# Kernel tuning notes

Hardware: AMD Instinct MI355X
Metric: run time of the kernel (lower is better)

The kernel has to match this reference:

```python
import jax, jax.numpy as jnp
import numpy as np

N = 100000          # nodes
E = 600000          # edges (avg degree ~6, mesh graph)
C_IN = 6            # input features (xyz + normals)
H = 64              # hidden channels per PointTransformerConv
OUT = 10            # out_channels
NEG_SLOPE = 0.01    # F.leaky_relu default slope
IN_DIMS = [C_IN, C_IN + H, C_IN + 2 * H, C_IN + 3 * H]


def _lin(key, fin, fout):
    return jax.random.normal(key, (fin, fout), jnp.float32) / np.float32(np.sqrt(fin))


def setup_inputs() -> dict:
    key = jax.random.key(0)
    ks = jax.random.split(key, 40)
    inp = {
        "x": jax.random.normal(ks[0], (N, C_IN), jnp.float32),
        "edge_index": jax.random.randint(ks[1], (2, E), 0, N, jnp.int32),
    }
    k = 2
    for l, fin in enumerate(IN_DIMS, start=1):
        inp[f"w{l}_lin"] = _lin(ks[k], fin, H); k += 1   # value projection (bias=False)
        inp[f"w{l}_src"] = _lin(ks[k], fin, H); k += 1   # attention src projection
        inp[f"w{l}_dst"] = _lin(ks[k], fin, H); k += 1   # attention dst projection
        inp[f"w{l}_pos"] = _lin(ks[k], fin, H); k += 1   # positional MLP (Linear)
        inp[f"b{l}_pos"] = jnp.zeros((H,), jnp.float32)
    inp["w_mlp1"] = _lin(ks[k], C_IN + 4 * H, H); k += 1
    inp["b_mlp1"] = jnp.zeros((H,), jnp.float32)
    inp["w_mlp2"] = _lin(ks[k], H, OUT); k += 1
    inp["b_mlp2"] = jnp.zeros((OUT,), jnp.float32)
    return inp


def _ptconv(x, src, dst, w_lin, w_src, w_dst, w_pos, b_pos):
    """PointTransformerConv with x serving as both features and positions.
    message = softmax_i(a_dst[i] - a_src[j] + delta_ij) * (h[j] + delta_ij),
    delta_ij = pos_nn(x_i - x_j); sum-aggregated over incoming edges."""
    h = x @ w_lin                                   # [N,H] values
    a_src = x @ w_src                               # [N,H]
    a_dst = x @ w_dst                               # [N,H]
    delta = (x[dst] - x[src]) @ w_pos + b_pos       # [E,H] pos_nn(pos_i - pos_j)
    alpha = a_dst[dst] - a_src[src] + delta         # [E,H] per-edge, per-channel logits
    # numerically stable segment softmax over edges grouped by destination node
    amax = jax.ops.segment_max(alpha, dst, num_segments=N)      # [N,H]
    e = jnp.exp(alpha - amax[dst])                              # [E,H]
    denom = jax.ops.segment_sum(e, dst, num_segments=N)         # [N,H]
    w = e / (denom[dst] + 1e-16)                                # [E,H]
    return jax.ops.segment_sum(w * (h[src] + delta), dst, num_segments=N)  # [N,H]


def _forward(x, edge_index, ps):
    src, dst = edge_index[0], edge_index[1]
    lrelu = lambda v: jnp.where(v > 0, v, NEG_SLOPE * v)
    x1 = _ptconv(x, src, dst, *ps[0])
    x2 = lrelu(_ptconv(jnp.concatenate([x, x1], 1), src, dst, *ps[1]))
    x3 = lrelu(_ptconv(jnp.concatenate([x, x1, x2], 1), src, dst, *ps[2]))
    x4 = lrelu(_ptconv(jnp.concatenate([x, x1, x2, x3], 1), src, dst, *ps[3]))
    out = jnp.concatenate([x, x1, x2, x3, x4], 1)   # [N, 262]
    w_mlp1, b_mlp1, w_mlp2, b_mlp2 = ps[4]
    out = out @ w_mlp1 + b_mlp1                     # dropout = identity (eval mode)
    return out @ w_mlp2 + b_mlp2                    # [N, OUT]


def reference(x, edge_index,
              w1_lin, w1_src, w1_dst, w1_pos, b1_pos,
              w2_lin, w2_src, w2_dst, w2_pos, b2_pos,
              w3_lin, w3_src, w3_dst, w3_pos, b3_pos,
              w4_lin, w4_src, w4_dst, w4_pos, b4_pos,
              w_mlp1, b_mlp1, w_mlp2, b_mlp2):
    ps = [(w1_lin, w1_src, w1_dst, w1_pos, b1_pos),
          (w2_lin, w2_src, w2_dst, w2_pos, b2_pos),
          (w3_lin, w3_src, w3_dst, w3_pos, b3_pos),
          (w4_lin, w4_src, w4_dst, w4_pos, b4_pos),
          (w_mlp1, b_mlp1, w_mlp2, b_mlp2)]
    return _forward(x, edge_index, ps)
```

## Files before the change

### kernel.cpp

```cpp
#include <hip/hip_runtime.h>
#include <hip/hip_fp16.h>

#define NN 100000
#define EE 600000
#define XSB 288
#define SCAN_B 2048
#define LOG2E 1.44269504f

typedef __attribute__((ext_vector_type(8))) short s16x8;
typedef __attribute__((ext_vector_type(4))) float f32x4;

__device__ inline unsigned short f2b(float f) {
    unsigned u = __float_as_uint(f);
    u += 0x7fffu + ((u >> 16) & 1u);
    return (unsigned short)(u >> 16);
}

__device__ inline void accum4(float* d, float* s, const uint4& r) {
    const unsigned* u = (const unsigned*)&r;
#pragma unroll
    for (int ch = 0; ch < 4; ch++) {
        d[ch] += __uint_as_float(u[ch] << 16);
        s[ch] += __uint_as_float(u[ch] & 0xFFFF0000u);
    }
}

__device__ inline void wconv_elem(int idx, int fin,
                                  const float* wlin, const float* wsrc,
                                  const float* wpos, unsigned short* wt) {
    int ks = idx / 6144;
    int rem = idx - ks * 6144;
    int col = rem >> 5, kk = rem & 31;
    int k = ks * 32 + kk;
    float val = 0.f;
    if (k < fin) {
        int m = col >> 6, c = col & 63;
        const float* W = (m == 0) ? wlin : (m == 1) ? wsrc : wpos;
        val = W[k * 64 + c];
    }
    wt[idx] = f2b(val);
}

#define O0 600000
#define O1 606144
#define O2 624576
#define O3 655296
#define O4 698304
#define O5 716736
#define O6 1316736
#define O7 1316800

__global__ __launch_bounds__(256) void k_setup(
    const float* __restrict__ x, const int* __restrict__ ei,
    const float* __restrict__ wl0, const float* __restrict__ ws0, const float* __restrict__ wp0,
    const float* __restrict__ wl1, const float* __restrict__ ws1, const float* __restrict__ wp1,
    const float* __restrict__ wl2, const float* __restrict__ ws2, const float* __restrict__ wp2,
    const float* __restrict__ wl3, const float* __restrict__ ws3, const float* __restrict__ wp3,
    const float* __restrict__ w1,
    unsigned short* __restrict__ xb,
    unsigned short* __restrict__ wt0, unsigned short* __restrict__ wt1,
    unsigned short* __restrict__ wt2, unsigned short* __restrict__ wt3,
    unsigned short* __restrict__ w1t, int* __restrict__ deg,
    unsigned* __restrict__ vgu) {
    int i = blockIdx.x * 256 + threadIdx.x;
    if (i < O0) {
        int n = i / 6, c = i - n * 6;
        xb[(size_t)n * XSB + c] = f2b(x[i]);
    } else if (i < O1) {
        wconv_elem(i - O0, 6, wl0, ws0, wp0, wt0);
    } else if (i < O2) {
        wconv_elem(i - O1, 70, wl1, ws1, wp1, wt1);
    } else if (i < O3) {
        wconv_elem(i - O2, 134, wl2, ws2, wp2, wt2);
    } else if (i < O4) {
        wconv_elem(i - O3, 198, wl3, ws3, wp3, wt3);
    } else if (i < O5) {
        int idx = i - O4;
        int col = idx / 288, k = idx - col * 288;
        w1t[idx] = f2b((k < 262) ? w1[k * 64 + col] : 0.f);
    } else if (i < O6) {
        atomicAdd(&deg[ei[EE + (i - O5)]], 1);
    } else if (i < O7) {
        vgu[(size_t)NN * 64 + (i - O6)] = 0u;
    }
}


__global__ void k_scan1(const int* __restrict__ deg, int* __restrict__ rowptr,
                        int* __restrict__ bsum) {
    __shared__ int sh[256];
    int b = blockIdx.x, t = threadIdx.x;
    int base = b * SCAN_B + t * 8;
    int vals[8];
    int s = 0;
#pragma unroll
    for (int j = 0; j < 8; j++) {
        int i = base + j;
        int d = (i < NN) ? deg[i] : 0;
        s += d;
        vals[j] = s;
    }
    sh[t] = s;
    __syncthreads();
    for (int off = 1; off < 256; off <<= 1) {
        int vv = (t >= off) ? sh[t - off] : 0;
        __syncthreads();
        sh[t] += vv;
        __syncthreads();
    }
    int excl = (t > 0) ? sh[t - 1] : 0;
#pragma unroll
    for (int j = 0; j < 8; j++) {
        int i = base + j;
        if (i < NN) rowptr[i + 1] = vals[j] + excl;
    }
    if (t == 255) bsum[b] = sh[255];
}

__global__ void k_scan3m(const int* __restrict__ deg, int* __restrict__ rowptr,
                         const int* __restrict__ bsum, int* __restrict__ cursor) {
    __shared__ int soff;
    int b = blockIdx.x, t = threadIdx.x;
    if (t < 64) {
        int v = (t < b) ? bsum[t] : 0;
#pragma unroll
        for (int m = 1; m < 64; m <<= 1) v += __shfl_xor(v, m);
        if (t == 0) soff = v;
    }
    __syncthreads();
    int off = soff;
    int base = b * SCAN_B + t * 8;
#pragma unroll
    for (int j = 0; j < 8; j++) {
        int i = base + j;
        if (i < NN) {
            int incl = rowptr[i + 1] + off;
            rowptr[i + 1] = incl;
            cursor[i] = incl - deg[i];
        }
    }
    if (b == 0 && t == 0) rowptr[0] = 0;
}

__global__ void k_scatter(const int* __restrict__ ei, int* __restrict__ cursor,
                          int* __restrict__ csrc) {
    int e = blockIdx.x * 256 + threadIdx.x;
    if (e < EE) {
        int d = ei[EE + e];
        int pos = atomicAdd(&cursor[d], 1);
        csrc[pos] = ei[e];
    }
}


template <int KP>
__global__ __launch_bounds__(256) void k_projm(
    const unsigned short* __restrict__ xb, const unsigned short* __restrict__ wt,
    const float* __restrict__ bpos,
    unsigned* __restrict__ vg, __half* __restrict__ qh) {
    __shared__ short wl[192 * 32];
    const int t = threadIdx.x;
    const int w = t >> 6, l = t & 63;
    const int lo = l & 15, hi = l >> 4;
    const int row_w = blockIdx.x * 128 + w * 32;

    f32x4 acc[2][12];
#pragma unroll
    for (int a = 0; a < 2; a++)
#pragma unroll
        for (int i = 0; i < 12; i++) acc[a][i] = (f32x4)0.f;

    const unsigned short* arow0 = xb + (size_t)(row_w + lo) * XSB;
    const unsigned short* arow1 = xb + (size_t)(row_w + 16 + lo) * XSB;
#pragma unroll
    for (int ks = 0; ks < KP / 32; ks++) {
        __syncthreads();
        {
            const uint4* src = (const uint4*)wt + (size_t)ks * 768;
            uint4* dst = (uint4*)wl;
#pragma unroll
            for (int i = 0; i < 3; i++) {
                int idx = i * 256 + t;
                dst[idx ^ ((idx >> 3) & 7)] = src[idx];
            }
        }
        __syncthreads();
        s16x8 af0 = *(const s16x8*)(arow0 + ks * 32 + hi * 8);
        s16x8 af1 = *(const s16x8*)(arow1 + ks * 32 + hi * 8);
#pragma unroll
        for (int ct = 0; ct < 12; ct++) {
            int ridx = (ct * 16 + lo) * 4 + hi;
            s16x8 bf = *(const s16x8*)&wl[(size_t)(ridx ^ ((ridx >> 3) & 7)) * 8];
            acc[0][ct] = __builtin_amdgcn_mfma_f32_16x16x32_bf16(af0, bf, acc[0][ct], 0, 0, 0);
            acc[1][ct] = __builtin_amdgcn_mfma_f32_16x16x32_bf16(af1, bf, acc[1][ct], 0, 0, 0);
        }
    }

#pragma unroll
    for (int tile = 0; tile < 2; tile++) {
#pragma unroll
        for (int r = 0; r < 4; r++) {
            int node = row_w + tile * 16 + hi * 4 + r;
            if (node < NN) {
#pragma unroll
                for (int j = 0; j < 4; j++) {
                    int c = j * 16 + lo;
                    float h  = acc[tile][0 + j][r];
                    float as = acc[tile][4 + j][r];
                    float p  = acc[tile][8 + j][r];
                    size_t o = (size_t)node * 64 + c;
                    float P = __builtin_amdgcn_exp2f(-(as + p) * LOG2E);
                    vg[o] = (unsigned)f2b(P) | ((unsigned)f2b(P * (h - p)) << 16);
                    qh[o] = __float2half(p + bpos[c]);
                }
            }
        }
    }
}


__global__ __launch_bounds__(256) void k_mlp1f(
    const unsigned short* __restrict__ xb, const unsigned short* __restrict__ w1t,
    const float* __restrict__ b1, const float* __restrict__ w2,
    const float* __restrict__ b2, float* __restrict__ out) {
    __shared__ float w2l[64][10];
    __shared__ float b2l[10];
    __shared__ float b1l[64];
    for (int t = threadIdx.x; t < 714; t += 256) {
        if (t < 640) ((float*)w2l)[t] = w2[t];
        else if (t < 650) b2l[t - 640] = b2[t - 640];
        else b1l[t - 650] = b1[t - 650];
    }
    __syncthreads();

    const int w = threadIdx.x >> 6, l = threadIdx.x & 63;
    const int lo = l & 15, hi = l >> 4;
    const int row_w = blockIdx.x * 256 + w * 64;

    f32x4 acc[4][4];
#pragma unroll
    for (int a = 0; a < 4; a++)
#pragma unroll
        for (int b = 0; b < 4; b++) acc[a][b] = (f32x4)0.f;

#pragma unroll
    for (int ks = 0; ks < 9; ks++) {
        const int k0 = ks * 32 + hi * 8;
        s16x8 bf[4];
#pragma unroll
        for (int ct = 0; ct < 4; ct++)
            bf[ct] = *(const s16x8*)(w1t + (size_t)(ct * 16 + lo) * 288 + k0);
#pragma unroll
        for (int rt = 0; rt < 4; rt++) {
            s16x8 af = *(const s16x8*)(xb + (size_t)(row_w + rt * 16 + lo) * XSB + k0);
#pragma unroll
            for (int ct = 0; ct < 4; ct++)
                acc[rt][ct] = __builtin_amdgcn_mfma_f32_16x16x32_bf16(af, bf[ct], acc[rt][ct], 0, 0, 0);
        }
    }

#pragma unroll
    for (int rt = 0; rt < 4; rt++) {
#pragma unroll
        for (int r = 0; r < 4; r++) {
            int node = row_w + rt * 16 + hi * 4 + r;
            float po[10];
#pragma unroll
            for (int o = 0; o < 10; o++) po[o] = 0.f;
#pragma unroll
            for (int ct = 0; ct < 4; ct++) {
                int c = ct * 16 + lo;
                float hv = acc[rt][ct][r] + b1l[c];
#pragma unroll
                for (int o = 0; o < 10; o++) po[o] = fmaf(hv, w2l[c][o], po[o]);
            }
#pragma unroll
            for (int m = 1; m < 16; m <<= 1)
#pragma unroll
                for (int o = 0; o < 10; o++) po[o] += __shfl_xor(po[o], m);
            if (lo == 0 && node < NN) {
                float* op = out + (size_t)node * 10;
#pragma unroll
                for (int o = 0; o < 5; o++)
                    *(float2*)(op + o * 2) = make_float2(po[o * 2] + b2l[o * 2],
                                                         po[o * 2 + 1] + b2l[o * 2 + 1]);
            }
        }
    }
}


template <int RELU>
__global__ __launch_bounds__(256) void k_edge(
    const uint4* __restrict__ vg,
    const uint2* __restrict__ qh,
    const int* __restrict__ rowptr, const int* __restrict__ csrc,
    unsigned short* __restrict__ xb, int col) {
    int l = threadIdx.x & 63;
    int g = l >> 4, lg = l & 15, gbase = g * 16;
    int node = (blockIdx.x * 4 + (threadIdx.x >> 6)) * 4 + g;
    int b = rowptr[node], e = rowptr[node + 1];
    int deg = e - b;
    int pre = (deg > 0) ? csrc[min(b + lg, e - 1)] : NN;
    uint2 qr = qh[(size_t)node * 16 + lg];
    float d[4] = {0.f, 0.f, 0.f, 0.f};
    float s[4] = {0.f, 0.f, 0.f, 0.f};

    int it = 0;
    int degc = min(deg, 16);
    for (; it < degc; it += 4) {
        int i0 = __shfl(pre, gbase + it);
        int i1 = (it + 1 < deg) ? __shfl(pre, gbase + it + 1) : NN;
        int i2 = (it + 2 < deg) ? __shfl(pre, gbase + it + 2) : NN;
        int i3 = (it + 3 < deg) ? __shfl(pre, gbase + it + 3) : NN;
        uint4 r0 = vg[(size_t)i0 * 16 + lg];
        uint4 r1 = vg[(size_t)i1 * 16 + lg];
        uint4 r2 = vg[(size_t)i2 * 16 + lg];
        uint4 r3 = vg[(size_t)i3 * 16 + lg];
        accum4(d, s, r0); accum4(d, s, r1); accum4(d, s, r2); accum4(d, s, r3);
    }
    for (; it < deg; ++it) {
        uint4 r0 = vg[(size_t)csrc[b + it] * 16 + lg];
        accum4(d, s, r0);
    }

    float2 q01 = __half22float2(*(const __half2*)&qr.x);
    float2 q23 = __half22float2(*(const __half2*)&qr.y);
    float qv[4] = {q01.x, q01.y, q23.x, q23.y};
    float o[4];
#pragma unroll
    for (int ch = 0; ch < 4; ch++) {
        float v = (s[ch] + qv[ch] * d[ch]) / (d[ch] + 1e-16f);
        if (RELU) v = (v > 0.f) ? v : 0.01f * v;
        o[ch] = v;
    }
    unsigned short* dst = xb + (size_t)node * XSB + col + 4 * lg;
    *(unsigned*)(dst)     = (unsigned)f2b(o[0]) | ((unsigned)f2b(o[1]) << 16);
    *(unsigned*)(dst + 2) = (unsigned)f2b(o[2]) | ((unsigned)f2b(o[3]) << 16);
}


extern "C" void kernel_launch(void* const* d_in, const int* in_sizes, int n_in,
                              void* d_out, int out_size, void* d_ws, size_t ws_size,
                              hipStream_t stream) {
    const float* x = (const float*)d_in[0];
    const int* ei = (const int*)d_in[1];
    const float* W[4][4];
    const float* BP[4];
    int base = 2;
    for (int l = 0; l < 4; l++) {
        for (int m = 0; m < 4; m++) W[l][m] = (const float*)d_in[base + m];
        BP[l] = (const float*)d_in[base + 4];
        base += 5;
    }
    const float* w1 = (const float*)d_in[22];
    const float* b1 = (const float*)d_in[23];
    const float* w2 = (const float*)d_in[24];
    const float* b2 = (const float*)d_in[25];

    char* wsp = (char*)d_ws;
    size_t off = 0;
    auto alloc = [&](size_t bytes) {
        void* p = wsp + off;
        off += (bytes + 255) & ~(size_t)255;
        return p;
    };
    unsigned short* xb = (unsigned short*)alloc((size_t)(NN + 256) * XSB * 2);
    unsigned* vg = (unsigned*)alloc((size_t)(NN + 1) * 64 * 4);
    __half* qh = (__half*)alloc((size_t)NN * 64 * 2);
    int* deg = (int*)alloc((size_t)NN * 4);
    int* rowptr = (int*)alloc((size_t)(NN + 1) * 4);
    int* cursor = (int*)alloc((size_t)NN * 4);
    int* bsum = (int*)alloc(1024 * 4);
    int* csrc = (int*)alloc((size_t)(EE + 16) * 4);
    const int KPv[4] = {32, 96, 160, 224};
    unsigned short* wt[4];
    for (int l = 0; l < 4; l++) wt[l] = (unsigned short*)alloc((size_t)192 * KPv[l] * 2);
    unsigned short* w1t = (unsigned short*)alloc((size_t)64 * 288 * 2);

    hipMemsetAsync(deg, 0, (size_t)NN * 4, stream);
    k_setup<<<(O7 + 255) / 256, 256, 0, stream>>>(
        x, ei, W[0][0], W[0][1], W[0][3], W[1][0], W[1][1], W[1][3],
        W[2][0], W[2][1], W[2][3], W[3][0], W[3][1], W[3][3], w1,
        xb, wt[0], wt[1], wt[2], wt[3], w1t, deg, vg);

    int nb = (NN + SCAN_B - 1) / SCAN_B;
    k_scan1<<<nb, 256, 0, stream>>>(deg, rowptr, bsum);
    k_scan3m<<<nb, 256, 0, stream>>>(deg, rowptr, bsum, cursor);
    k_scatter<<<(EE + 255) / 256, 256, 0, stream>>>(ei, cursor, csrc);

    const int gProj = (NN + 127) / 128;
    const int gEdge = NN / 16;
    const uint4* vgu = (const uint4*)vg;
    const uint2* qh2 = (const uint2*)qh;

    k_projm<32><<<gProj, 256, 0, stream>>>(xb, wt[0], BP[0], vg, qh);
    k_edge<0><<<gEdge, 256, 0, stream>>>(vgu, qh2, rowptr, csrc, xb, 6);
    k_projm<96><<<gProj, 256, 0, stream>>>(xb, wt[1], BP[1], vg, qh);
    k_edge<1><<<gEdge, 256, 0, stream>>>(vgu, qh2, rowptr, csrc, xb, 70);
    k_projm<160><<<gProj, 256, 0, stream>>>(xb, wt[2], BP[2], vg, qh);
    k_edge<1><<<gEdge, 256, 0, stream>>>(vgu, qh2, rowptr, csrc, xb, 134);
    k_projm<224><<<gProj, 256, 0, stream>>>(xb, wt[3], BP[3], vg, qh);
    k_edge<1><<<gEdge, 256, 0, stream>>>(vgu, qh2, rowptr, csrc, xb, 198);

    k_mlp1f<<<(NN + 255) / 256, 256, 0, stream>>>(xb, w1t, b1, w2, b2, (float*)d_out);
}
```

Measured before the change: 295.6 us.

## Fuse layer-1 projection into setup and align feature columns to 32

The first-layer projection (K=6) now runs inside the setup kernel with scalar FMAs, so the separate k_projm<32> launch is dropped. The bf16 feature buffer layout changes so raw x occupies columns 0-31 (zero-padded) and each layer's output starts at an aligned column (32, 96, 160, 224); weight transposes remap rows to match. The edge kernel's output store becomes a single 8-byte vector store. This saves one launch and gives aligned vector stores, but the setup kernel now does more work per thread (zero-padding, per-node projection).

New measurement: 302.4 us. 1.02x slower.

```diff
diff --git a/kernel.cpp b/kernel.cpp
--- a/kernel.cpp
+++ b/kernel.cpp
@@ -32,42 +32,63 @@
     int rem = idx - ks * 6144;
     int col = rem >> 5, kk = rem & 31;
     int k = ks * 32 + kk;
+    int row = (k < 6) ? k : k - 26;
     float val = 0.f;
-    if (k < fin) {
+    if (k < 6 || (k >= 32 && row < fin)) {
         int m = col >> 6, c = col & 63;
         const float* W = (m == 0) ? wlin : (m == 1) ? wsrc : wpos;
-        val = W[k * 64 + c];
+        val = W[row * 64 + c];
     }
     wt[idx] = f2b(val);
 }
 
-#define O0 600000
-#define O1 606144
-#define O2 624576
-#define O3 655296
-#define O4 698304
-#define O5 716736
-#define O6 1316736
-#define O7 1316800
+#define O0 3200000
+#define O1 3600000
+#define O2 3618432
+#define O3 3649152
+#define O4 3692160
+#define O5 3710592
+#define O6 4310592
+#define O7 4310656
 
 __global__ __launch_bounds__(256) void k_setup(
     const float* __restrict__ x, const int* __restrict__ ei,
     const float* __restrict__ wl0, const float* __restrict__ ws0, const float* __restrict__ wp0,
+    const float* __restrict__ bp0,
     const float* __restrict__ wl1, const float* __restrict__ ws1, const float* __restrict__ wp1,
     const float* __restrict__ wl2, const float* __restrict__ ws2, const float* __restrict__ wp2,
     const float* __restrict__ wl3, const float* __restrict__ ws3, const float* __restrict__ wp3,
     const float* __restrict__ w1,
     unsigned short* __restrict__ xb,
-    unsigned short* __restrict__ wt0, unsigned short* __restrict__ wt1,
-    unsigned short* __restrict__ wt2, unsigned short* __restrict__ wt3,
+    unsigned short* __restrict__ wt1, unsigned short* __restrict__ wt2,
+    unsigned short* __restrict__ wt3,
     unsigned short* __restrict__ w1t, int* __restrict__ deg,
-    unsigned* __restrict__ vgu) {
+    unsigned* __restrict__ vg, __half* __restrict__ qh) {
     int i = blockIdx.x * 256 + threadIdx.x;
     if (i < O0) {
-        int n = i / 6, c = i - n * 6;
-        xb[(size_t)n * XSB + c] = f2b(x[i]);
+        int n = i >> 5, c = i & 31;
+        xb[(size_t)n * XSB + c] = (c < 6) ? f2b(x[n * 6 + c]) : (unsigned short)0;
     } else if (i < O1) {
-        wconv_elem(i - O0, 6, wl0, ws0, wp0, wt0);
+        int idx = i - O0;
+        int node = idx >> 2, cg = (idx & 3) * 16;
+        float xr[6];
+#pragma unroll
+        for (int j = 0; j < 6; j++) xr[j] = x[node * 6 + j];
+#pragma unroll
+        for (int cc = 0; cc < 16; cc++) {
+            int c = cg + cc;
+            float h = 0.f, as = 0.f, p = 0.f;
+#pragma unroll
+            for (int j = 0; j < 6; j++) {
+                h  = fmaf(xr[j], wl0[j * 64 + c], h);
+                as = fmaf(xr[j], ws0[j * 64 + c], as);
+                p  = fmaf(xr[j], wp0[j * 64 + c], p);
+            }
+            size_t o = (size_t)node * 64 + c;
+            float P = __builtin_amdgcn_exp2f(-(as + p) * LOG2E);
+            vg[o] = (unsigned)f2b(P) | ((unsigned)f2b(P * (h - p)) << 16);
+            qh[o] = __float2half(p + bp0[c]);
+        }
     } else if (i < O2) {
         wconv_elem(i - O1, 70, wl1, ws1, wp1, wt1);
     } else if (i < O3) {
@@ -77,11 +98,13 @@
     } else if (i < O5) {
         int idx = i - O4;
         int col = idx / 288, k = idx - col * 288;
-        w1t[idx] = f2b((k < 262) ? w1[k * 64 + col] : 0.f);
+        int row = (k < 6) ? k : k - 26;
+        bool valid = (k < 6) || (k >= 32 && row < 262);
+        w1t[idx] = f2b(valid ? w1[row * 64 + col] : 0.f);
     } else if (i < O6) {
         atomicAdd(&deg[ei[EE + (i - O5)]], 1);
     } else if (i < O7) {
-        vgu[(size_t)NN * 64 + (i - O6)] = 0u;
+        vg[(size_t)NN * 64 + (i - O6)] = 0u;
     }
 }
 
@@ -334,9 +357,9 @@
         if (RELU) v = (v > 0.f) ? v : 0.01f * v;
         o[ch] = v;
     }
-    unsigned short* dst = xb + (size_t)node * XSB + col + 4 * lg;
-    *(unsigned*)(dst)     = (unsigned)f2b(o[0]) | ((unsigned)f2b(o[1]) << 16);
-    *(unsigned*)(dst + 2) = (unsigned)f2b(o[2]) | ((unsigned)f2b(o[3]) << 16);
+    unsigned p01 = (unsigned)f2b(o[0]) | ((unsigned)f2b(o[1]) << 16);
+    unsigned p23 = (unsigned)f2b(o[2]) | ((unsigned)f2b(o[3]) << 16);
+    *(uint2*)(xb + (size_t)node * XSB + col + 4 * lg) = make_uint2(p01, p23);
 }
 
 
@@ -373,16 +396,19 @@
     int* cursor = (int*)alloc((size_t)NN * 4);
     int* bsum = (int*)alloc(1024 * 4);
     int* csrc = (int*)alloc((size_t)(EE + 16) * 4);
-    const int KPv[4] = {32, 96, 160, 224};
-    unsigned short* wt[4];
-    for (int l = 0; l < 4; l++) wt[l] = (unsigned short*)alloc((size_t)192 * KPv[l] * 2);
+    const int KPv[3] = {96, 160, 224};
+    unsigned short* wt[3];
+    for (int l = 0; l < 3; l++) wt[l] = (unsigned short*)alloc((size_t)192 * KPv[l] * 2);
     unsigned short* w1t = (unsigned short*)alloc((size_t)64 * 288 * 2);
 
     hipMemsetAsync(deg, 0, (size_t)NN * 4, stream);
     k_setup<<<(O7 + 255) / 256, 256, 0, stream>>>(
-        x, ei, W[0][0], W[0][1], W[0][3], W[1][0], W[1][1], W[1][3],
-        W[2][0], W[2][1], W[2][3], W[3][0], W[3][1], W[3][3], w1,
-        xb, wt[0], wt[1], wt[2], wt[3], w1t, deg, vg);
+        x, ei,
+        W[0][0], W[0][1], W[0][3], BP[0],
+        W[1][0], W[1][1], W[1][3],
+        W[2][0], W[2][1], W[2][3],
+        W[3][0], W[3][1], W[3][3], w1,
+        xb, wt[0], wt[1], wt[2], w1t, deg, vg, qh);
 
     int nb = (NN + SCAN_B - 1) / SCAN_B;
     k_scan1<<<nb, 256, 0, stream>>>(deg, rowptr, bsum);
@@ -394,14 +420,13 @@
     const uint4* vgu = (const uint4*)vg;
     const uint2* qh2 = (const uint2*)qh;
 
-    k_projm<32><<<gProj, 256, 0, stream>>>(xb, wt[0], BP[0], vg, qh);
-    k_edge<0><<<gEdge, 256, 0, stream>>>(vgu, qh2, rowptr, csrc, xb, 6);
-    k_projm<96><<<gProj, 256, 0, stream>>>(xb, wt[1], BP[1], vg, qh);
-    k_edge<1><<<gEdge, 256, 0, stream>>>(vgu, qh2, rowptr, csrc, xb, 70);
-    k_projm<160><<<gProj, 256, 0, stream>>>(xb, wt[2], BP[2], vg, qh);
-    k_edge<1><<<gEdge, 256, 0, stream>>>(vgu, qh2, rowptr, csrc, xb, 134);
-    k_projm<224><<<gProj, 256, 0, stream>>>(xb, wt[3], BP[3], vg, qh);
-    k_edge<1><<<gEdge, 256, 0, stream>>>(vgu, qh2, rowptr, csrc, xb, 198);
+    k_edge<0><<<gEdge, 256, 0, stream>>>(vgu, qh2, rowptr, csrc, xb, 32);
+    k_projm<96><<<gProj, 256, 0, stream>>>(xb, wt[0], BP[1], vg, qh);
+    k_edge<1><<<gEdge, 256, 0, stream>>>(vgu, qh2, rowptr, csrc, xb, 96);
+    k_projm<160><<<gProj, 256, 0, stream>>>(xb, wt[1], BP[2], vg, qh);
+    k_edge<1><<<gEdge, 256, 0, stream>>>(vgu, qh2, rowptr, csrc, xb, 160);
+    k_projm<224><<<gProj, 256, 0, stream>>>(xb, wt[2], BP[3], vg, qh);
+    k_edge<1><<<gEdge, 256, 0, stream>>>(vgu, qh2, rowptr, csrc, xb, 224);
 
     k_mlp1f<<<(NN + 255) / 256, 256, 0, stream>>>(xb, w1t, b1, w2, b2, (float*)d_out);
 }
```
